# Kernel optimization log

Measured on AMD Instinct MI355X. Metric: run time of the kernel, lower is better.

## Reference

```python
import jax, jax.numpy as jnp
import numpy as np

B, IN, OUT, N, K = 2048, 4096, 4096, 64, 4  # batch, in_features, out_features, num_nodes, degree


def setup_inputs() -> dict:
    key = jax.random.key(0)
    k0, k1, k2, k3 = jax.random.split(key, 4)
    x = jax.random.normal(k0, (B, IN), dtype=jnp.float32)
    # kaiming-ish init for the linear weight
    W = jax.random.normal(k1, (OUT, IN), dtype=jnp.float32) * (1.0 / np.sqrt(IN))
    ecoeff = jax.random.uniform(k2, (N, N), dtype=jnp.float32, minval=0.1, maxval=0.5)
    phase = jax.random.uniform(k3, (N, N), dtype=jnp.float32, minval=0.0, maxval=2.0 * np.pi)
    tension = jnp.ones((N,), dtype=jnp.float32)
    # deterministic degree-K ring topology: paths[i] = [(i+1..i+K) % N]
    src = jnp.repeat(jnp.arange(N), K).astype(jnp.int32)            # [E]
    dst = ((src + jnp.tile(jnp.arange(1, K + 1), N)) % N).astype(jnp.int32)  # [E]
    return {"x": x, "W": W, "ecoeff": ecoeff, "phase": phase,
            "tension": tension, "src": src, "dst": dst}


def reference(x, W, ecoeff, phase, tension, src, dst):
    # EntangledConnectionLayer.forward
    b = x.shape[0]
    out_features = W.shape[0]
    n = tension.shape[0]
    opn = out_features // n  # out_per_node

    out = x @ W.T  # [B, OUT] == F.linear(x, weights)
    nodes = out.reshape(b, n, opn)  # [B, N, opn] node-sliced view of output

    # entangled_connection_function on a real signal:
    # real(sig * (1 + eps*exp(i*phi)) / (1 + tau_i*tau_j)) = sig*(1+eps*cos(phi))/(1+tau_i*tau_j)
    eps = ecoeff[src, dst]                    # [E]
    phi = phase[src, dst]                     # [E]
    tau = tension[src] * tension[dst]         # [E]
    scale = (1.0 + eps * jnp.cos(phi)) / (1.0 + tau)  # [E]

    contrib = nodes[:, src, :] * scale[None, :, None]  # [B, E, opn]
    entangled = jnp.zeros_like(nodes).at[:, dst, :].add(contrib)  # scatter-add over edges

    return out + 0.5 * entangled.reshape(b, out_features)
```

## Files before the change

### kernel.cpp

```cpp
#include <hip/hip_runtime.h>
#include <hip/hip_bf16.h>

#define TILE 128
#define BK   64

#define BM8 128
#define BN8 256
#define BK8 64

typedef __attribute__((ext_vector_type(8))) short bf16x8;
typedef __attribute__((ext_vector_type(4))) float f32x4;

__device__ __forceinline__ unsigned short f32_to_bf16(float f) {
    unsigned u = __float_as_uint(f);
    unsigned rounded = u + 0x7FFF + ((u >> 16) & 1);
    return (unsigned short)(rounded >> 16);
}
__device__ __forceinline__ float bf16_to_f32(unsigned short h) {
    return __uint_as_float(((unsigned)h) << 16);
}
__device__ __forceinline__ bool probe_f32(const void* tens) {
    return ((const unsigned short*)tens)[0] == 0;
}

__global__ __launch_bounds__(256)
void prep_kernel(const void* __restrict__ xv, const void* __restrict__ Wv,
                 const void* __restrict__ ecoeff, const void* __restrict__ phase,
                 const void* __restrict__ tens,
                 const int* __restrict__ srcIdx, const int* __restrict__ dstIdx,
                 unsigned short* __restrict__ xa, unsigned short* __restrict__ wp,
                 int E, int K, int castB)
{
    constexpr int NODES = 64, CHUNK = 256, CAP = 8;
    __shared__ unsigned short buf[NODES * CHUNK];
    __shared__ int   cnt[NODES];
    __shared__ int   slist[NODES * CAP];
    __shared__ float clist[NODES * CAP];

    const bool isF32 = probe_f32(tens);
    const int tid = threadIdx.x;
    const int b   = blockIdx.x;

    if (b < castB) {
        const size_t i = ((size_t)b * 256 + tid) * 8;
        if (isF32) {
            const float4 a = *(const float4*)((const float*)xv + i);
            const float4 c = *(const float4*)((const float*)xv + i + 4);
            unsigned short p[8];
            p[0]=f32_to_bf16(a.x); p[1]=f32_to_bf16(a.y); p[2]=f32_to_bf16(a.z); p[3]=f32_to_bf16(a.w);
            p[4]=f32_to_bf16(c.x); p[5]=f32_to_bf16(c.y); p[6]=f32_to_bf16(c.z); p[7]=f32_to_bf16(c.w);
            *(bf16x8*)(xa + i) = *(const bf16x8*)p;
        } else {
            *(bf16x8*)(xa + i) = *(const bf16x8*)((const unsigned short*)xv + i);
        }
        return;
    }

    const int wb = b - castB;
    const int j  = wb & 63;
    const int k0 = (wb >> 6) * CHUNK;

    if (tid < NODES) cnt[tid] = 0;
    __syncthreads();
    if (tid < E) {
        const int s = srcIdx[tid];
        const int d = dstIdx[tid];
        float eps, phi, ts, td;
        if (isF32) {
            eps = ((const float*)ecoeff)[s * NODES + d];
            phi = ((const float*)phase)[s * NODES + d];
            ts  = ((const float*)tens)[s];
            td  = ((const float*)tens)[d];
        } else {
            eps = bf16_to_f32(((const unsigned short*)ecoeff)[s * NODES + d]);
            phi = bf16_to_f32(((const unsigned short*)phase)[s * NODES + d]);
            ts  = bf16_to_f32(((const unsigned short*)tens)[s]);
            td  = bf16_to_f32(((const unsigned short*)tens)[d]);
        }
        const float coef = 0.5f * (1.0f + eps * __cosf(phi)) / (1.0f + ts * td);
        const int pos = atomicAdd(&cnt[d], 1);
        if (pos < CAP) { slist[d * CAP + pos] = s; clist[d * CAP + pos] = coef; }
    }

    if (isF32) {
        for (int idx = tid; idx < NODES * CHUNK / 4; idx += 256) {
            const int s = idx >> 6;
            const int p = idx & 63;
            const float4 v = *(const float4*)
                ((const float*)Wv + (size_t)(s * 64 + j) * K + k0 + p * 4);
            ushort4 u;
            u.x = f32_to_bf16(v.x); u.y = f32_to_bf16(v.y);
            u.z = f32_to_bf16(v.z); u.w = f32_to_bf16(v.w);
            *(ushort4*)&buf[s * CHUNK + p * 4] = u;
        }
    } else {
        for (int idx = tid; idx < NODES * CHUNK / 4; idx += 256) {
            const int s = idx >> 6;
            const int p = idx & 63;
            *(ushort4*)&buf[s * CHUNK + p * 4] = *(const ushort4*)
                ((const unsigned short*)Wv + (size_t)(s * 64 + j) * K + k0 + p * 4);
        }
    }
    __syncthreads();

    const int kk4  = (tid & 63) * 4;
    const int dgrp = (tid >> 6) * 16;
#pragma unroll 4
    for (int dd = 0; dd < 16; ++dd) {
        const int d = dgrp + dd;
        const ushort4 a = *(const ushort4*)&buf[d * CHUNK + kk4];
        float v0 = bf16_to_f32(a.x), v1 = bf16_to_f32(a.y);
        float v2 = bf16_to_f32(a.z), v3 = bf16_to_f32(a.w);
        const int n = cnt[d] < CAP ? cnt[d] : CAP;
        for (int t = 0; t < n; ++t) {
            const float c = clist[d * CAP + t];
            const ushort4 s4 = *(const ushort4*)&buf[slist[d * CAP + t] * CHUNK + kk4];
            v0 += c * bf16_to_f32(s4.x); v1 += c * bf16_to_f32(s4.y);
            v2 += c * bf16_to_f32(s4.z); v3 += c * bf16_to_f32(s4.w);
        }
        ushort4 o;
        o.x = f32_to_bf16(v0); o.y = f32_to_bf16(v1);
        o.z = f32_to_bf16(v2); o.w = f32_to_bf16(v3);
        *(ushort4*)(wp + (size_t)(d * 64 + j) * K + k0 + kk4) = o;
    }
}

#define GLOAD(g, l) __builtin_amdgcn_global_load_lds( \
        (__attribute__((address_space(1))) const void*)(g), \
        (__attribute__((address_space(3))) void*)(l), 16, 0, 0)

__global__ __launch_bounds__(512)
void gemm8_kernel(const unsigned short* __restrict__ A,
                  const unsigned short* __restrict__ B,
                  void* __restrict__ Cv, const void* __restrict__ tens,
                  int M, int N, int K)
{
    __shared__ __align__(16) unsigned short As[3][BM8 * BK8];
    __shared__ __align__(16) unsigned short Bs[3][BN8 * BK8];

    const bool isF32 = probe_f32(tens);
    asm volatile("" :: "v"((int)isF32));

    const int tid  = threadIdx.x;
    const int lane = tid & 63;
    const int w    = tid >> 6;
    const int wm   = (w >> 2) * 64;
    const int wn   = (w & 3) * 64;
    const int m0   = blockIdx.y * BM8;
    const int n0   = blockIdx.x * BN8;

    const int rsub = lane >> 3;
    const int csw  = ((lane & 7) ^ rsub) * 8;
    const int arow0 = w * 16;
    const int brow0 = w * 32;

    const unsigned short* aSrc = A + (size_t)(m0 + arow0 + rsub) * K + csw;
    const unsigned short* bSrc = B + (size_t)(n0 + brow0 + rsub) * K + csw;

    const int rr  = lane & 15;
    const int kq  = lane >> 4;
    const int sw7 = rr & 7;
    const int sl0 = (kq ^ sw7) * 8;
    const int sl1 = ((4 + kq) ^ sw7) * 8;

    f32x4 acc[4][4] = {};

    const int NT = K / BK8;

#define STAGE_ALL(kt, bi) do { \
        const unsigned short* as_ = aSrc + (size_t)(kt) * BK8; \
        const unsigned short* bs_ = bSrc + (size_t)(kt) * BK8; \
        GLOAD(as_,                  &As[bi][(arow0     ) * BK8]); \
        GLOAD(as_ + (size_t)8 * K,  &As[bi][(arow0 +  8) * BK8]); \
        GLOAD(bs_,                  &Bs[bi][(brow0     ) * BK8]); \
        GLOAD(bs_ + (size_t)8  * K, &Bs[bi][(brow0 +  8) * BK8]); \
        GLOAD(bs_ + (size_t)16 * K, &Bs[bi][(brow0 + 16) * BK8]); \
        GLOAD(bs_ + (size_t)24 * K, &Bs[bi][(brow0 + 24) * BK8]); \
    } while (0)

    STAGE_ALL(0, 0);
    STAGE_ALL(1, 1);
    asm volatile("s_waitcnt vmcnt(6)" ::: "memory");
    __builtin_amdgcn_s_barrier();
    __builtin_amdgcn_sched_barrier(0);

    int cur = 0;
    for (int t = 0; t < NT; ++t) {
        int nb = cur + 2; if (nb >= 3) nb -= 3;
        const bool pf = (t + 2 < NT);
        const unsigned short* asC = &As[cur][0];
        const unsigned short* bsC = &Bs[cur][0];

        bf16x8 av0[4], bv0[4], av1[4], bv1[4];
#pragma unroll
        for (int i = 0; i < 4; ++i)
            av0[i] = *(const bf16x8*)&asC[(wm + i * 16 + rr) * BK8 + sl0];
#pragma unroll
        for (int i = 0; i < 4; ++i)
            bv0[i] = *(const bf16x8*)&bsC[(wn + i * 16 + rr) * BK8 + sl0];
#pragma unroll
        for (int i = 0; i < 4; ++i)
            av1[i] = *(const bf16x8*)&asC[(wm + i * 16 + rr) * BK8 + sl1];
#pragma unroll
        for (int i = 0; i < 4; ++i)
            bv1[i] = *(const bf16x8*)&bsC[(wn + i * 16 + rr) * BK8 + sl1];

        if (pf) STAGE_ALL(t + 2, nb);

        asm volatile("s_waitcnt lgkmcnt(0)" ::: "memory");
        __builtin_amdgcn_sched_barrier(0);

        __builtin_amdgcn_s_setprio(1);
#pragma unroll
        for (int mt = 0; mt < 4; ++mt)
#pragma unroll
            for (int nc = 0; nc < 4; ++nc)
                acc[mt][nc] = __builtin_amdgcn_mfma_f32_16x16x32_bf16(
                    av0[mt], bv0[nc], acc[mt][nc], 0, 0, 0);
#pragma unroll
        for (int mt = 0; mt < 4; ++mt)
#pragma unroll
            for (int nc = 0; nc < 4; ++nc)
                acc[mt][nc] = __builtin_amdgcn_mfma_f32_16x16x32_bf16(
                    av1[mt], bv1[nc], acc[mt][nc], 0, 0, 0);
        __builtin_amdgcn_s_setprio(0);

        if (pf)                 asm volatile("s_waitcnt vmcnt(6)" ::: "memory");
        else if (t + 1 < NT)    asm volatile("s_waitcnt vmcnt(0)" ::: "memory");
        __builtin_amdgcn_s_barrier();
        __builtin_amdgcn_sched_barrier(0);

        cur = cur + 1; if (cur == 3) cur = 0;
    }

    const int quad = (lane >> 4) * 4;
    const int col  = lane & 15;
#pragma unroll
    for (int mt = 0; mt < 4; ++mt)
#pragma unroll
        for (int nc = 0; nc < 4; ++nc)
#pragma unroll
            for (int r = 0; r < 4; ++r) {
                const size_t gr = (size_t)(m0 + wm + mt * 16 + quad + r);
                const size_t gc = (size_t)(n0 + wn + nc * 16 + col);
                const float v = acc[mt][nc][r];
                if (isF32) ((float*)Cv)[gr * N + gc] = v;
                else       ((unsigned short*)Cv)[gr * N + gc] = f32_to_bf16(v);
            }
}

__global__ __launch_bounds__(256)
void gemm_bt_kernel(const void* __restrict__ Av, const void* __restrict__ Bv,
                    void* __restrict__ Cv, const void* __restrict__ tens,
                    int M, int N, int K)
{
    __shared__ __align__(16) short As[TILE * BK];
    __shared__ __align__(16) short Bs[TILE * BK];

    const bool isF32 = probe_f32(tens);
    const int tid  = threadIdx.x;
    const int lane = tid & 63;
    const int w    = tid >> 6;
    const int wm   = (w >> 1) * 64;
    const int wn   = (w & 1) * 64;
    const int m0   = blockIdx.y * TILE;
    const int n0   = blockIdx.x * TILE;
    f32x4 acc[4][4] = {};
    const int lrow = lane >> 3;
    const int lcol = (lane & 7) * 8;

    for (int k0 = 0; k0 < K; k0 += BK) {
        if (!isF32) {
            const short* A = (const short*)Av;
            const short* B = (const short*)Bv;
#pragma unroll
            for (int t = 0; t < 4; ++t) {
                const int br = t * 32 + w * 8;
                const short* ga = A + (size_t)(m0 + br + lrow) * K + (k0 + lcol);
                const short* gb = B + (size_t)(n0 + br + lrow) * K + (k0 + lcol);
                __builtin_amdgcn_global_load_lds(
                    (__attribute__((address_space(1))) const void*)ga,
                    (__attribute__((address_space(3))) void*)&As[br * BK], 16, 0, 0);
                __builtin_amdgcn_global_load_lds(
                    (__attribute__((address_space(1))) const void*)gb,
                    (__attribute__((address_space(3))) void*)&Bs[br * BK], 16, 0, 0);
            }
        } else {
            const float* A = (const float*)Av;
            const float* B = (const float*)Bv;
#pragma unroll
            for (int t = 0; t < 4; ++t) {
                const int br = t * 32 + w * 8;
                const int row = br + lrow;
                const float* ga = A + (size_t)(m0 + row) * K + (k0 + lcol);
                const float* gb = B + (size_t)(n0 + row) * K + (k0 + lcol);
                float4 a0 = *(const float4*)(ga);
                float4 a1 = *(const float4*)(ga + 4);
                float4 b0 = *(const float4*)(gb);
                float4 b1 = *(const float4*)(gb + 4);
                short pa[8], pb[8];
                pa[0]=f32_to_bf16(a0.x); pa[1]=f32_to_bf16(a0.y);
                pa[2]=f32_to_bf16(a0.z); pa[3]=f32_to_bf16(a0.w);
                pa[4]=f32_to_bf16(a1.x); pa[5]=f32_to_bf16(a1.y);
                pa[6]=f32_to_bf16(a1.z); pa[7]=f32_to_bf16(a1.w);
                pb[0]=f32_to_bf16(b0.x); pb[1]=f32_to_bf16(b0.y);
                pb[2]=f32_to_bf16(b0.z); pb[3]=f32_to_bf16(b0.w);
                pb[4]=f32_to_bf16(b1.x); pb[5]=f32_to_bf16(b1.y);
                pb[6]=f32_to_bf16(b1.z); pb[7]=f32_to_bf16(b1.w);
                *(bf16x8*)&As[row * BK + lcol] = *(const bf16x8*)pa;
                *(bf16x8*)&Bs[row * BK + lcol] = *(const bf16x8*)pb;
            }
        }
        __syncthreads();
#pragma unroll
        for (int kk = 0; kk < BK; kk += 32) {
            const int rk = kk + (lane >> 4) * 8;
            const int rr = lane & 15;
            bf16x8 av[4], bv[4];
#pragma unroll
            for (int i = 0; i < 4; ++i)
                av[i] = *(const bf16x8*)&As[(wm + i * 16 + rr) * BK + rk];
#pragma unroll
            for (int i = 0; i < 4; ++i)
                bv[i] = *(const bf16x8*)&Bs[(wn + i * 16 + rr) * BK + rk];
#pragma unroll
            for (int mt = 0; mt < 4; ++mt)
#pragma unroll
                for (int nt = 0; nt < 4; ++nt)
                    acc[mt][nt] = __builtin_amdgcn_mfma_f32_16x16x32_bf16(
                        av[mt], bv[nt], acc[mt][nt], 0, 0, 0);
        }
        __syncthreads();
    }
    const int quad = (lane >> 4) * 4;
    const int col  = lane & 15;
#pragma unroll
    for (int mt = 0; mt < 4; ++mt)
#pragma unroll
        for (int nt = 0; nt < 4; ++nt)
#pragma unroll
            for (int r = 0; r < 4; ++r) {
                const size_t gr = (size_t)(m0 + wm + mt * 16 + quad + r);
                const size_t gc = (size_t)(n0 + wn + nt * 16 + col);
                const float v = acc[mt][nt][r];
                if (isF32) ((float*)Cv)[gr * N + gc] = v;
                else       ((unsigned short*)Cv)[gr * N + gc] = f32_to_bf16(v);
            }
}

__global__ __launch_bounds__(256)
void entangle_kernel(void* __restrict__ Cv,
                     const void* __restrict__ ecoeff,
                     const void* __restrict__ phase,
                     const void* __restrict__ tens,
                     const int* __restrict__ srcIdx,
                     const int* __restrict__ dstIdx,
                     int E)
{
    constexpr int NODES = 64, OPN = 64, FEAT = 4096, ROWS = 2, CAP = 8;
    __shared__ float rows[ROWS * FEAT];
    __shared__ int   cnt[NODES];
    __shared__ int   slist[NODES * CAP];
    __shared__ float clist[NODES * CAP];

    const bool isF32 = probe_f32(tens);
    const int tid = threadIdx.x;
    if (tid < NODES) cnt[tid] = 0;
    __syncthreads();

    if (tid < E) {
        const int s = srcIdx[tid];
        const int d = dstIdx[tid];
        float eps, phi, ts, td;
        if (isF32) {
            eps = ((const float*)ecoeff)[s * NODES + d];
            phi = ((const float*)phase)[s * NODES + d];
            ts  = ((const float*)tens)[s];
            td  = ((const float*)tens)[d];
        } else {
            eps = bf16_to_f32(((const unsigned short*)ecoeff)[s * NODES + d]);
            phi = bf16_to_f32(((const unsigned short*)phase)[s * NODES + d]);
            ts  = bf16_to_f32(((const unsigned short*)tens)[s]);
            td  = bf16_to_f32(((const unsigned short*)tens)[d]);
        }
        const float coef = 0.5f * (1.0f + eps * __cosf(phi)) / (1.0f + ts * td);
        const int pos = atomicAdd(&cnt[d], 1);
        if (pos < CAP) { slist[d * CAP + pos] = s; clist[d * CAP + pos] = coef; }
    }

    const size_t row0 = (size_t)blockIdx.x * ROWS;
    if (isF32) {
        const float4* g = (const float4*)((const float*)Cv + row0 * FEAT);
        float4* l = (float4*)rows;
        for (int i = tid; i < ROWS * FEAT / 4; i += 256) l[i] = g[i];
    } else {
        const ushort2* g = (const ushort2*)((const unsigned short*)Cv + row0 * FEAT);
        for (int i = tid; i < ROWS * FEAT / 2; i += 256) {
            const ushort2 u = g[i];
            rows[i * 2 + 0] = bf16_to_f32(u.x);
            rows[i * 2 + 1] = bf16_to_f32(u.y);
        }
    }
    __syncthreads();

    for (int c = 0; c < ROWS * FEAT / 256; ++c) {
        const int i = c * 256 + tid;
        const int r = i >> 12;
        const int o = i & (FEAT - 1);
        const int d = o >> 6;
        const int j = o & (OPN - 1);
        float v = rows[i];
        const int n = cnt[d] < CAP ? cnt[d] : CAP;
        for (int t = 0; t < n; ++t)
            v += clist[d * CAP + t] * rows[(r << 12) + slist[d * CAP + t] * OPN + j];
        if (isF32) ((float*)Cv)[(row0 + r) * FEAT + o] = v;
        else       ((unsigned short*)Cv)[(row0 + r) * FEAT + o] = f32_to_bf16(v);
    }
}

extern "C" void kernel_launch(void* const* d_in, const int* in_sizes, int n_in,
                              void* d_out, int out_size, void* d_ws, size_t ws_size,
                              hipStream_t stream)
{
    const void* x       = d_in[0];
    const void* W       = d_in[1];
    const void* ecoeff  = d_in[2];
    const void* phase   = d_in[3];
    const void* tension = d_in[4];
    const int*  src     = (const int*)d_in[5];
    const int*  dst     = (const int*)d_in[6];

    const int INF  = 4096;
    const int OUTF = 4096;
    const int M    = in_sizes[0] / INF;
    const int E    = in_sizes[5];

    const size_t needA = (size_t)M * INF * sizeof(unsigned short);
    const size_t needW = (size_t)OUTF * INF * sizeof(unsigned short);

    if (ws_size >= needA + needW && (M % BM8) == 0) {
        unsigned short* xa = (unsigned short*)d_ws;
        unsigned short* wp = (unsigned short*)((char*)d_ws + needA);

        const int castB = (M * INF) / (256 * 8);
        const int wpB   = 64 * (INF / 256);
        prep_kernel<<<dim3(castB + wpB), dim3(256), 0, stream>>>(
            x, W, ecoeff, phase, tension, src, dst, xa, wp, E, INF, castB);
        gemm8_kernel<<<dim3(OUTF / BN8, M / BM8), dim3(512), 0, stream>>>(
            xa, wp, d_out, tension, M, OUTF, INF);
    } else {
        dim3 grid(OUTF / TILE, M / TILE), block(256);
        gemm_bt_kernel<<<grid, block, 0, stream>>>(x, W, d_out, tension, M, OUTF, INF);
        entangle_kernel<<<dim3(M / 2), block, 0, stream>>>(
            d_out, ecoeff, phase, tension, src, dst, E);
    }
}
```

Baseline: 218.7 us.

## Shrink GEMM tile to 128x128x32 with 4 waves and re-derive LDS swizzle

Changes the bf16 MFMA GEMM from 128x256 tiles with BK=64 and 8 waves to 128x128 tiles with BK=32 and 4 waves per block. The global-to-LDS load mapping, XOR swizzle and wait counts are rewritten to fit the narrower K tile. Each iteration now issues one MFMA pass instead of two. The smaller LDS footprint and block double the grid and may allow more blocks per CU, at the cost of lower per-block data reuse and more barriers per unit of K.

```diff
diff --git a/kernel.cpp b/kernel.cpp
--- a/kernel.cpp
+++ b/kernel.cpp
@@ -5,8 +5,8 @@
 #define BK   64
 
 #define BM8 128
-#define BN8 256
-#define BK8 64
+#define BN8 128
+#define BK8 32
 
 typedef __attribute__((ext_vector_type(8))) short bf16x8;
 typedef __attribute__((ext_vector_type(4))) float f32x4;
@@ -129,7 +129,7 @@
         (__attribute__((address_space(1))) const void*)(g), \
         (__attribute__((address_space(3))) void*)(l), 16, 0, 0)
 
-__global__ __launch_bounds__(512)
+__global__ __launch_bounds__(256)
 void gemm8_kernel(const unsigned short* __restrict__ A,
                   const unsigned short* __restrict__ B,
                   void* __restrict__ Cv, const void* __restrict__ tens,
@@ -144,24 +144,21 @@
     const int tid  = threadIdx.x;
     const int lane = tid & 63;
     const int w    = tid >> 6;
-    const int wm   = (w >> 2) * 64;
-    const int wn   = (w & 3) * 64;
+    const int wm   = (w >> 1) * 64;
+    const int wn   = (w & 1) * 64;
     const int m0   = blockIdx.y * BM8;
     const int n0   = blockIdx.x * BN8;
 
-    const int rsub = lane >> 3;
-    const int csw  = ((lane & 7) ^ rsub) * 8;
-    const int arow0 = w * 16;
-    const int brow0 = w * 32;
-
-    const unsigned short* aSrc = A + (size_t)(m0 + arow0 + rsub) * K + csw;
-    const unsigned short* bSrc = B + (size_t)(n0 + brow0 + rsub) * K + csw;
+    const int rsub = lane >> 2;
+    const int csw  = ((lane & 3) ^ ((lane >> 3) & 3)) * 8;
+    const int row0 = w * 32;
+
+    const unsigned short* aSrc = A + (size_t)(m0 + row0 + rsub) * K + csw;
+    const unsigned short* bSrc = B + (size_t)(n0 + row0 + rsub) * K + csw;
 
     const int rr  = lane & 15;
     const int kq  = lane >> 4;
-    const int sw7 = rr & 7;
-    const int sl0 = (kq ^ sw7) * 8;
-    const int sl1 = ((4 + kq) ^ sw7) * 8;
+    const int slt = (kq ^ ((rr >> 1) & 3)) * 8;
 
     f32x4 acc[4][4] = {};
 
@@ -170,17 +167,15 @@
 #define STAGE_ALL(kt, bi) do { \
         const unsigned short* as_ = aSrc + (size_t)(kt) * BK8; \
         const unsigned short* bs_ = bSrc + (size_t)(kt) * BK8; \
-        GLOAD(as_,                  &As[bi][(arow0     ) * BK8]); \
-        GLOAD(as_ + (size_t)8 * K,  &As[bi][(arow0 +  8) * BK8]); \
-        GLOAD(bs_,                  &Bs[bi][(brow0     ) * BK8]); \
-        GLOAD(bs_ + (size_t)8  * K, &Bs[bi][(brow0 +  8) * BK8]); \
-        GLOAD(bs_ + (size_t)16 * K, &Bs[bi][(brow0 + 16) * BK8]); \
-        GLOAD(bs_ + (size_t)24 * K, &Bs[bi][(brow0 + 24) * BK8]); \
+        GLOAD(as_,                  &As[bi][(row0     ) * BK8]); \
+        GLOAD(as_ + (size_t)16 * K, &As[bi][(row0 + 16) * BK8]); \
+        GLOAD(bs_,                  &Bs[bi][(row0     ) * BK8]); \
+        GLOAD(bs_ + (size_t)16 * K, &Bs[bi][(row0 + 16) * BK8]); \
     } while (0)
 
     STAGE_ALL(0, 0);
     STAGE_ALL(1, 1);
-    asm volatile("s_waitcnt vmcnt(6)" ::: "memory");
+    asm volatile("s_waitcnt vmcnt(4)" ::: "memory");
     __builtin_amdgcn_s_barrier();
     __builtin_amdgcn_sched_barrier(0);
 
@@ -191,19 +186,13 @@
         const unsigned short* asC = &As[cur][0];
         const unsigned short* bsC = &Bs[cur][0];
 
-        bf16x8 av0[4], bv0[4], av1[4], bv1[4];
+        bf16x8 av[4], bv[4];
 #pragma unroll
         for (int i = 0; i < 4; ++i)
-            av0[i] = *(const bf16x8*)&asC[(wm + i * 16 + rr) * BK8 + sl0];
+            av[i] = *(const bf16x8*)&asC[(wm + i * 16 + rr) * BK8 + slt];
 #pragma unroll
         for (int i = 0; i < 4; ++i)
-            bv0[i] = *(const bf16x8*)&bsC[(wn + i * 16 + rr) * BK8 + sl0];
-#pragma unroll
-        for (int i = 0; i < 4; ++i)
-            av1[i] = *(const bf16x8*)&asC[(wm + i * 16 + rr) * BK8 + sl1];
-#pragma unroll
-        for (int i = 0; i < 4; ++i)
-            bv1[i] = *(const bf16x8*)&bsC[(wn + i * 16 + rr) * BK8 + sl1];
+            bv[i] = *(const bf16x8*)&bsC[(wn + i * 16 + rr) * BK8 + slt];
 
         if (pf) STAGE_ALL(t + 2, nb);
 
@@ -216,16 +205,10 @@
 #pragma unroll
             for (int nc = 0; nc < 4; ++nc)
                 acc[mt][nc] = __builtin_amdgcn_mfma_f32_16x16x32_bf16(
-                    av0[mt], bv0[nc], acc[mt][nc], 0, 0, 0);
-#pragma unroll
-        for (int mt = 0; mt < 4; ++mt)
-#pragma unroll
-            for (int nc = 0; nc < 4; ++nc)
-                acc[mt][nc] = __builtin_amdgcn_mfma_f32_16x16x32_bf16(
-                    av1[mt], bv1[nc], acc[mt][nc], 0, 0, 0);
+                    av[mt], bv[nc], acc[mt][nc], 0, 0, 0);
         __builtin_amdgcn_s_setprio(0);
 
-        if (pf)                 asm volatile("s_waitcnt vmcnt(6)" ::: "memory");
+        if (pf)                 asm volatile("s_waitcnt vmcnt(4)" ::: "memory");
         else if (t + 1 < NT)    asm volatile("s_waitcnt vmcnt(0)" ::: "memory");
         __builtin_amdgcn_s_barrier();
         __builtin_amdgcn_sched_barrier(0);
@@ -446,7 +429,7 @@
         const int wpB   = 64 * (INF / 256);
         prep_kernel<<<dim3(castB + wpB), dim3(256), 0, stream>>>(
             x, W, ecoeff, phase, tension, src, dst, xa, wp, E, INF, castB);
-        gemm8_kernel<<<dim3(OUTF / BN8, M / BM8), dim3(512), 0, stream>>>(
+        gemm8_kernel<<<dim3(OUTF / BN8, M / BM8), dim3(256), 0, stream>>>(
             xa, wp, d_out, tension, M, OUTF, INF);
     } else {
         dim3 grid(OUTF / TILE, M / TILE), block(256);
```

Result: no change. 220.9 us (+1.0%).
